# Kernel tuning notes

Hardware: AMD Instinct MI355X
Metric: run time of the kernel (lower is better)

The kernel has to match this reference:

```python
import math
import jax, jax.numpy as jnp
import numpy as np

E = 24  # num experts


def layer_norm(x, w, b, eps=1e-6):
    m = x.mean(-1, keepdims=True)
    v = x.var(-1, keepdims=True)
    return (x - m) / jnp.sqrt(v + eps) * w + b


def top2_dispatch(x, Wg, C):
    # x: [S, d] -> combine/dispatch: [S, E, C] (GShard/DeepSpeed top-2 gating)
    logits = x @ Wg                                   # [S, E]
    gates = jax.nn.softmax(logits, axis=-1)
    idx1 = jnp.argmax(gates, axis=-1)
    m1 = jax.nn.one_hot(idx1, E, dtype=x.dtype)       # [S, E]
    masked = jnp.where(m1 > 0, -jnp.inf, logits)
    idx2 = jnp.argmax(masked, axis=-1)
    m2 = jax.nn.one_hot(idx2, E, dtype=x.dtype)
    # position of each token within its expert's capacity buffer
    loc1 = jnp.cumsum(m1, axis=0) - m1
    loc2 = jnp.cumsum(m2, axis=0) - m2 + jnp.sum(m1, axis=0, keepdims=True)
    m1 = m1 * (loc1 < C)                              # drop overflow tokens
    m2 = m2 * (loc2 < C)
    g1 = jnp.sum(gates * m1, axis=-1)
    g2 = jnp.sum(gates * m2, axis=-1)
    denom = jnp.maximum(g1 + g2, 1e-9)
    g1, g2 = g1 / denom, g2 / denom
    p1 = jnp.sum(loc1 * m1, axis=-1).astype(jnp.int32)
    p2 = jnp.sum(loc2 * m2, axis=-1).astype(jnp.int32)
    c1 = g1[:, None, None] * m1[:, :, None] * jax.nn.one_hot(p1, C, dtype=x.dtype)[:, None, :]
    c2 = g2[:, None, None] * m2[:, :, None] * jax.nn.one_hot(p2, C, dtype=x.dtype)[:, None, :]
    combine = c1 + c2                                  # [S, E, C]
    dispatch = (combine > 0).astype(x.dtype)
    return combine, dispatch


def moe_apply(x, combine, dispatch, W, b):
    # dispatch tokens to expert buffers, per-expert GEMM, combine back
    disp = jnp.einsum('sec,sd->ecd', dispatch, x)      # [E, C, d]
    h = jnp.einsum('ecd,edf->ecf', disp, W) + b[:, None, :]
    return jnp.einsum('sec,ecf->sf', combine, h)       # [S, f]


def setup_inputs() -> dict:
    b, seq, d_in, d_hid = 4, 2048, 1024, 4096
    ks = jax.random.split(jax.random.key(0), 6)
    s = 0.02
    return {
        'x': jax.random.normal(ks[0], (b, seq, d_in), dtype=jnp.float32),
        'Wg': jax.random.normal(ks[1], (d_in, E), dtype=jnp.float32) * s,
        'W1': jax.random.normal(ks[2], (E, d_in, d_hid), dtype=jnp.float32) * s,
        'b1': jnp.zeros((E, d_hid), dtype=jnp.float32),
        'W2': jax.random.normal(ks[3], (E, d_hid, d_in), dtype=jnp.float32) * s,
        'b2': jnp.zeros((E, d_in), dtype=jnp.float32),
        'ln_hid_w': jnp.ones((4, d_hid), dtype=jnp.float32),
        'ln_hid_b': jnp.zeros((4, d_hid), dtype=jnp.float32),
        'ln_out_w': jnp.ones((d_in,), dtype=jnp.float32),
        'ln_out_b': jnp.zeros((d_in,), dtype=jnp.float32),
    }


def reference(x, Wg, W1, b1, W2, b2, ln_hid_w, ln_hid_b, ln_out_w, ln_out_b):
    bsz, seq, d = x.shape
    H = 4
    n = seq // H
    S = bsz * n  # tokens per sub-sequence MoE call
    C = math.ceil(2 * S / E)  # top-2 capacity, capacity_factor=1.0
    # b (h n) c -> h (b n) c
    xg = x.reshape(bsz, H, n, d).transpose(1, 0, 2, 3).reshape(H, S, d)

    def per_group(xf, lw, lb):
        combine, dispatch = top2_dispatch(xf, Wg, C)
        h = moe_apply(xf, combine, dispatch, W1, b1)       # [S, d_hid]
        h = layer_norm(h, lw, lb)
        h = jax.nn.relu(h)                                  # dropout = identity (eval)
        return moe_apply(h, combine, dispatch, W2, b2)      # reuse gate_decision

    out = jax.vmap(per_group)(xg, ln_hid_w, ln_hid_b)       # [H, S, d]
    out = out.reshape(H, bsz, n, d).transpose(1, 0, 2, 3).reshape(bsz, seq, d)
    return layer_norm(out + x, ln_out_w, ln_out_b)
```

## Files before the change

### kernel.cpp

```cpp
#include <hip/hip_runtime.h>
#include <cstdint>
#include <cstddef>

#define E_      24
#define D_IN    1024
#define D_HID   4096
#define HGRP    4
#define BSZ     4
#define SEQ     2048
#define NSUB    512
#define S_      2048
#define NTOKG   8192
#define CAP     171
#define MR      768
#define MTILE   3
#define KSPL2   4

typedef __attribute__((ext_vector_type(4))) float          f32x4;
typedef __attribute__((ext_vector_type(4))) unsigned short u16x4;
typedef __attribute__((ext_vector_type(8))) unsigned short u16x8;
typedef __attribute__((ext_vector_type(4))) unsigned int   u32x4;
typedef __attribute__((ext_vector_type(8))) short          s16x8;

__device__ __forceinline__ unsigned short f2bf(float f) {
  unsigned int u = __float_as_uint(f);
  u += 0x7fffu + ((u >> 16) & 1u);
  return (unsigned short)(u >> 16);
}
__device__ __forceinline__ float bf2f(unsigned short v) {
  return __uint_as_float(((unsigned int)v) << 16);
}

__global__ __launch_bounds__(64)
void k_gating(const float* __restrict__ x, const float* __restrict__ Wg,
              int* __restrict__ tokE1, int* __restrict__ tokE2,
              float* __restrict__ tokG1, float* __restrict__ tokG2) {
  int tg = blockIdx.x;
  int h = tg >> 11, s = tg & 2047;
  int bi = s >> 9, ni = s & 511;
  const float* xr = x + ((size_t)bi*SEQ + (size_t)h*NSUB + ni) * D_IN;
  int lane = threadIdx.x;
  float acc[E_];
  #pragma unroll
  for (int e = 0; e < E_; ++e) acc[e] = 0.f;
  #pragma unroll
  for (int it = 0; it < D_IN/256; ++it) {
    f32x4 xv = *(const f32x4*)(xr + it*256 + lane*4);
    #pragma unroll
    for (int j = 0; j < 4; ++j) {
      float xs = xv[j];
      const float* wrow = Wg + (size_t)(it*256 + lane*4 + j) * E_;
      #pragma unroll
      for (int e = 0; e < E_; ++e) acc[e] += xs * wrow[e];
    }
  }
  #pragma unroll
  for (int e = 0; e < E_; ++e) {
    float v = acc[e];
    v += __shfl_xor(v, 32); v += __shfl_xor(v, 16); v += __shfl_xor(v, 8);
    v += __shfl_xor(v, 4);  v += __shfl_xor(v, 2);  v += __shfl_xor(v, 1);
    acc[e] = v;
  }
  if (lane == 0) {
    float mx = acc[0];
    #pragma unroll
    for (int e = 1; e < E_; ++e) mx = fmaxf(mx, acc[e]);
    float den = 0.f;
    #pragma unroll
    for (int e = 0; e < E_; ++e) den += expf(acc[e] - mx);
    int i1 = 0; float v1 = acc[0];
    #pragma unroll
    for (int e = 1; e < E_; ++e) if (acc[e] > v1) { v1 = acc[e]; i1 = e; }
    int i2 = -1; float v2 = -3.4e38f;
    #pragma unroll
    for (int e = 0; e < E_; ++e) if (e != i1 && acc[e] > v2) { v2 = acc[e]; i2 = e; }
    tokE1[tg] = i1; tokE2[tg] = i2;
    tokG1[tg] = expf(v1 - mx) / den;
    tokG2[tg] = expf(v2 - mx) / den;
  }
}

__global__ void k_init_slots(int* __restrict__ slotTok) {
  slotTok[blockIdx.x*256 + threadIdx.x] = -1;
}

__global__ __launch_bounds__(64)
void k_scan(const int* __restrict__ tokE1, const int* __restrict__ tokE2,
            float* __restrict__ tokG1, float* __restrict__ tokG2,
            int* __restrict__ tokP1, int* __restrict__ tokP2,
            int* __restrict__ slotTok) {
  int h = blockIdx.x;
  int lane = threadIdx.x;
  __shared__ int cnt[64][E_];
  __shared__ int tot1[E_];
  const int CH = S_/64;
  const int* e1 = tokE1 + h*S_;
  const int* e2 = tokE2 + h*S_;
  #pragma unroll
  for (int e = 0; e < E_; ++e) cnt[lane][e] = 0;
  __syncthreads();
  for (int k = 0; k < CH; ++k) cnt[lane][e1[lane*CH + k]]++;
  __syncthreads();
  if (lane < E_) {
    int run = 0;
    for (int j = 0; j < 64; ++j) { int t = cnt[j][lane]; cnt[j][lane] = run; run += t; }
    tot1[lane] = run;
  }
  __syncthreads();
  for (int k = 0; k < CH; ++k) {
    int s = lane*CH + k;
    int e = e1[s];
    int p = cnt[lane][e]++;
    int tg = h*S_ + s;
    if (p < CAP) { tokP1[tg] = p; slotTok[e*MR + h*CAP + p] = tg; }
    else         { tokP1[tg] = -1; }
  }
  __syncthreads();
  #pragma unroll
  for (int e = 0; e < E_; ++e) cnt[lane][e] = 0;
  __syncthreads();
  for (int k = 0; k < CH; ++k) cnt[lane][e2[lane*CH + k]]++;
  __syncthreads();
  if (lane < E_) {
    int run = tot1[lane];
    for (int j = 0; j < 64; ++j) { int t = cnt[j][lane]; cnt[j][lane] = run; run += t; }
  }
  __syncthreads();
  for (int k = 0; k < CH; ++k) {
    int s = lane*CH + k;
    int e = e2[s];
    int p = cnt[lane][e]++;
    int tg = h*S_ + s;
    if (p < CAP) { tokP2[tg] = p; slotTok[e*MR + h*CAP + p] = tg; }
    else         { tokP2[tg] = -1; }
  }
  __syncthreads();
  for (int k = 0; k < CH; ++k) {
    int tg = h*S_ + k*64 + lane;
    float g1 = (tokP1[tg] >= 0) ? tokG1[tg] : 0.f;
    float g2 = (tokP2[tg] >= 0) ? tokG2[tg] : 0.f;
    float den = fmaxf(g1 + g2, 1e-9f);
    tokG1[tg] = g1 / den;
    tokG2[tg] = g2 / den;
  }
}

__global__ __launch_bounds__(256)
void k_gather1(const float* __restrict__ x, const int* __restrict__ slotTok,
               unsigned short* __restrict__ A1) {
  int row = blockIdx.x;
  int tok = slotTok[row];
  int t = threadIdx.x;
  int k = t*4;
  int ba = ((k & 63)*2) ^ ((row & 7) << 4);
  char* dst = (char*)A1 + (size_t)row*(D_IN*2) + (size_t)(k >> 6)*128 + ba;
  u16x4 pk;
  if (tok >= 0) {
    int h = tok >> 11, s = tok & 2047;
    int bi = s >> 9, ni = s & 511;
    const float* xr = x + ((size_t)bi*SEQ + (size_t)h*NSUB + ni) * D_IN;
    f32x4 v = *(const f32x4*)(xr + k);
    pk.x = f2bf(v.x); pk.y = f2bf(v.y); pk.z = f2bf(v.z); pk.w = f2bf(v.w);
  } else {
    pk.x = 0; pk.y = 0; pk.z = 0; pk.w = 0;
  }
  *(u16x4*)dst = pk;
}

template<int K, int N>
__global__ __launch_bounds__(256)
void k_cvtW(const float* __restrict__ W, unsigned short* __restrict__ Wt) {
  const int NB = N/64, KB = K/64;
  int bid = blockIdx.x;
  int kb = bid % KB;
  int rem = bid / KB;
  int nb = rem % NB;
  int e  = rem / NB;
  __shared__ float lds[64][65];
  int t = threadIdx.x;
  int rl = t >> 4;
  int cl = (t & 15) * 4;
  const float* base = W + ((size_t)e*K + (size_t)kb*64)*N + (size_t)nb*64;
  #pragma unroll
  for (int p = 0; p < 4; ++p) {
    int r = p*16 + rl;
    f32x4 v = *(const f32x4*)(base + (size_t)r*N + cl);
    lds[cl+0][r] = v.x; lds[cl+1][r] = v.y; lds[cl+2][r] = v.z; lds[cl+3][r] = v.w;
  }
  __syncthreads();
  int nl = t >> 2, kg = (t & 3) * 16;
  u16x8 c0, c1;
  #pragma unroll
  for (int j = 0; j < 8; ++j) {
    c0[j] = f2bf(lds[nl][kg + j]);
    c1[j] = f2bf(lds[nl][kg + 8 + j]);
  }
  char* dst = (char*)Wt + ((size_t)e*N + (size_t)nb*64 + nl)*(K*2) + (size_t)kb*128;
  int sw = (nl & 7) << 4;
  *(u16x8*)(dst + ((kg*2)      ^ sw)) = c0;
  *(u16x8*)(dst + ((kg*2 + 16) ^ sw)) = c1;
}

template<int KROW, int KCHUNK, int N>
__global__ __launch_bounds__(512, 2)
void k_gemm(const unsigned short* __restrict__ A, const unsigned short* __restrict__ Wt,
            const float* __restrict__ bias, unsigned short* __restrict__ Out) {
  const int NT = N / 256;
  const int KSPLIT = KROW / KCHUNK;
  const int NKT = KCHUNK / 64;
  int cpx = gridDim.x >> 3;
  int lb = blockIdx.x;
  int bid = (lb & 7) * cpx + (lb >> 3);
  int mt  = bid % MTILE;
  int rem = bid / MTILE;
  int kc  = rem % KSPLIT;
  rem /= KSPLIT;
  int nt  = rem % NT;
  int e   = rem / NT;

  const char* Ab = (const char*)A  + ((size_t)e*MR + (size_t)mt*256) * (KROW*2);
  const char* Bb = (const char*)Wt + ((size_t)e*N  + (size_t)nt*256) * (KROW*2);
  size_t kbase = (size_t)kc * (KCHUNK*2);

  __shared__ unsigned short As0[256*64];
  __shared__ unsigned short As1[256*64];
  __shared__ unsigned short Bs0[256*64];
  __shared__ unsigned short Bs1[256*64];

  int tid  = threadIdx.x;
  int lane = tid & 63;
  int wid  = tid >> 6;
  int wr = wid >> 2, wc = wid & 3;

  f32x4 acc[8][4];
  #pragma unroll
  for (int i = 0; i < 8; ++i)
    #pragma unroll
    for (int j = 0; j < 4; ++j) acc[i][j] = (f32x4)0.f;

  auto stageAi = [&](int kt2, unsigned short* As, int i) {
    size_t koff = kbase + (size_t)kt2*128;
    int L = i*8192 + tid*16;
    __builtin_amdgcn_global_load_lds(
        (const __attribute__((address_space(1))) void*)(Ab + (size_t)(L >> 7)*(KROW*2) + koff + (L & 127)),
        (__attribute__((address_space(3))) void*)((char*)As + L), 16, 0, 0);
  };
  auto stageBi = [&](int kt2, unsigned short* Bs, int i) {
    size_t koff = kbase + (size_t)kt2*128;
    int L = i*8192 + tid*16;
    __builtin_amdgcn_global_load_lds(
        (const __attribute__((address_space(1))) void*)(Bb + (size_t)(L >> 7)*(KROW*2) + koff + (L & 127)),
        (__attribute__((address_space(3))) void*)((char*)Bs + L), 16, 0, 0);
  };
  auto fragsA = [&](const unsigned short* As, int ra, int ks, s16x8* afr) {
    int kb = ks*64 + (lane >> 4)*16;
    #pragma unroll
    for (int i = 0; i < 4; ++i) {
      int r = wr*128 + ra*64 + i*16 + (lane & 15);
      afr[i] = *(const s16x8*)((const char*)As + r*128 + (kb ^ ((r & 7) << 4)));
    }
  };
  auto fragsB = [&](const unsigned short* Bs, int ks, s16x8* bfr) {
    int kb = ks*64 + (lane >> 4)*16;
    #pragma unroll
    for (int j = 0; j < 4; ++j) {
      int c = wc*64 + j*16 + (lane & 15);
      bfr[j] = *(const s16x8*)((const char*)Bs + c*128 + (kb ^ ((c & 7) << 4)));
    }
  };
  auto mfma16 = [&](int ra, const s16x8* afr, const s16x8* bfr) {
    __builtin_amdgcn_s_setprio(1);
    #pragma unroll
    for (int i = 0; i < 4; ++i)
      #pragma unroll
      for (int j = 0; j < 4; ++j)
        acc[ra*4+i][j] = __builtin_amdgcn_mfma_f32_16x16x32_bf16(afr[i], bfr[j], acc[ra*4+i][j], 0, 0, 0);
    __builtin_amdgcn_s_setprio(0);
  };

  unsigned short *Acur = As0, *Anxt = As1, *Bcur = Bs0, *Bnxt = Bs1;

  stageBi(0, Bcur, 0); stageBi(0, Bcur, 1); stageBi(0, Bcur, 2); stageBi(0, Bcur, 3);
  stageAi(0, Acur, 0); stageAi(0, Acur, 2);
  stageAi(0, Acur, 1); stageAi(0, Acur, 3);
  asm volatile("s_waitcnt vmcnt(2)" ::: "memory");
  __builtin_amdgcn_sched_barrier(0);
  __builtin_amdgcn_s_barrier();

  for (int kt = 0; kt < NKT; ++kt) {
    int tn = (kt + 1 < NKT) ? kt + 1 : kt;
    s16x8 afr[4], bfr[4];
    fragsA(Acur, 0, 0, afr); fragsB(Bcur, 0, bfr);
    stageBi(tn, Bnxt, 0); stageBi(tn, Bnxt, 1);
    asm volatile("s_waitcnt vmcnt(2)" ::: "memory");
    __builtin_amdgcn_sched_barrier(0);
    __builtin_amdgcn_s_barrier();
    asm volatile("s_waitcnt lgkmcnt(0)" ::: "memory");
    __builtin_amdgcn_sched_barrier(0);
    mfma16(0, afr, bfr);
    __builtin_amdgcn_s_barrier();
    fragsA(Acur, 1, 0, afr);
    stageBi(tn, Bnxt, 2); stageBi(tn, Bnxt, 3);
    __builtin_amdgcn_s_barrier();
    asm volatile("s_waitcnt lgkmcnt(0)" ::: "memory");
    __builtin_amdgcn_sched_barrier(0);
    mfma16(1, afr, bfr);
    __builtin_amdgcn_s_barrier();
    fragsA(Acur, 0, 1, afr); fragsB(Bcur, 1, bfr);
    stageAi(tn, Anxt, 0); stageAi(tn, Anxt, 2);
    __builtin_amdgcn_s_barrier();
    asm volatile("s_waitcnt lgkmcnt(0)" ::: "memory");
    __builtin_amdgcn_sched_barrier(0);
    mfma16(0, afr, bfr);
    __builtin_amdgcn_s_barrier();
    fragsA(Acur, 1, 1, afr);
    stageAi(tn, Anxt, 1); stageAi(tn, Anxt, 3);
    __builtin_amdgcn_s_barrier();
    asm volatile("s_waitcnt lgkmcnt(0)" ::: "memory");
    __builtin_amdgcn_sched_barrier(0);
    mfma16(1, afr, bfr);
    asm volatile("s_waitcnt vmcnt(2)" ::: "memory");
    __builtin_amdgcn_sched_barrier(0);
    __builtin_amdgcn_s_barrier();
    unsigned short* t1 = Acur; Acur = Anxt; Anxt = t1;
    unsigned short* t2 = Bcur; Bcur = Bnxt; Bnxt = t2;
  }

  unsigned short* Op = Out + (size_t)kc * ((size_t)E_*MR*N);
  #pragma unroll
  for (int j = 0; j < 4; ++j) {
    int col = nt*256 + wc*64 + j*16 + (lane & 15);
    float bv = (kc == 0) ? bias[(size_t)e*N + col] : 0.f;
    #pragma unroll
    for (int i = 0; i < 8; ++i) {
      int rowb = mt*256 + wr*128 + i*16 + (lane >> 4)*4;
      #pragma unroll
      for (int r = 0; r < 4; ++r) {
        float v = acc[i][j][r] + bv;
        Op[(size_t)e*MR*N + (size_t)(rowb + r)*N + col] = f2bf(v);
      }
    }
  }
}

__global__ __launch_bounds__(256)
void k_zero_empty(const int* __restrict__ slotTok, unsigned short* __restrict__ A2) {
  int row = blockIdx.x;
  if (slotTok[row] >= 0) return;
  u32x4 z = (u32x4)0u;
  char* base = (char*)A2 + (size_t)row*(D_HID*2) + threadIdx.x*32;
  *(u32x4*)base = z;
  *(u32x4*)(base + 16) = z;
}

__global__ __launch_bounds__(256)
void k_combine_ln(const unsigned short* __restrict__ H1,
                  const int* __restrict__ tokE1, const int* __restrict__ tokE2,
                  const int* __restrict__ tokP1, const int* __restrict__ tokP2,
                  const float* __restrict__ tokG1, const float* __restrict__ tokG2,
                  const float* __restrict__ lnw, const float* __restrict__ lnb,
                  unsigned short* __restrict__ A2) {
  int tg = blockIdx.x;
  int h = tg >> 11;
  int p1 = tokP1[tg], p2 = tokP2[tg];
  if (p1 < 0 && p2 < 0) return;
  float g1 = tokG1[tg], g2 = tokG2[tg];
  long r1 = (p1 >= 0) ? ((long)tokE1[tg]*MR + h*CAP + p1) : -1;
  long r2 = (p2 >= 0) ? ((long)tokE2[tg]*MR + h*CAP + p2) : -1;
  int t = threadIdx.x;
  float v[16];
  float sum = 0.f, sq = 0.f;
  #pragma unroll
  for (int u = 0; u < 4; ++u) {
    int f = u*1024 + t*4;
    float a0 = 0.f, a1 = 0.f, a2 = 0.f, a3 = 0.f;
    if (r1 >= 0) {
      u16x4 q = *(const u16x4*)(H1 + (size_t)r1*D_HID + f);
      a0 += g1*bf2f(q.x); a1 += g1*bf2f(q.y); a2 += g1*bf2f(q.z); a3 += g1*bf2f(q.w);
    }
    if (r2 >= 0) {
      u16x4 q = *(const u16x4*)(H1 + (size_t)r2*D_HID + f);
      a0 += g2*bf2f(q.x); a1 += g2*bf2f(q.y); a2 += g2*bf2f(q.z); a3 += g2*bf2f(q.w);
    }
    v[u*4+0] = a0; v[u*4+1] = a1; v[u*4+2] = a2; v[u*4+3] = a3;
    sum += a0 + a1 + a2 + a3;
    sq  += a0*a0 + a1*a1 + a2*a2 + a3*a3;
  }
  #pragma unroll
  for (int o = 32; o; o >>= 1) { sum += __shfl_xor(sum, o); sq += __shfl_xor(sq, o); }
  __shared__ float redA[4], redB[4];
  int wid = t >> 6;
  if ((t & 63) == 0) { redA[wid] = sum; redB[wid] = sq; }
  __syncthreads();
  float S = redA[0] + redA[1] + redA[2] + redA[3];
  float Q = redB[0] + redB[1] + redB[2] + redB[3];
  float m = S * (1.f / D_HID);
  float var = Q * (1.f / D_HID) - m*m;
  float rs = rsqrtf(var + 1e-6f);
  #pragma unroll
  for (int u = 0; u < 4; ++u) {
    int f = u*1024 + t*4;
    u16x4 pk;
    float y0 = fmaxf((v[u*4+0]-m)*rs*lnw[h*D_HID+f+0] + lnb[h*D_HID+f+0], 0.f);
    float y1 = fmaxf((v[u*4+1]-m)*rs*lnw[h*D_HID+f+1] + lnb[h*D_HID+f+1], 0.f);
    float y2 = fmaxf((v[u*4+2]-m)*rs*lnw[h*D_HID+f+2] + lnb[h*D_HID+f+2], 0.f);
    float y3 = fmaxf((v[u*4+3]-m)*rs*lnw[h*D_HID+f+3] + lnb[h*D_HID+f+3], 0.f);
    pk.x = f2bf(y0); pk.y = f2bf(y1); pk.z = f2bf(y2); pk.w = f2bf(y3);
    int chunk = f >> 6;
    int ob = (f & 63)*2;
    if (r1 >= 0)
      *(u16x4*)((char*)A2 + (size_t)r1*(D_HID*2) + (size_t)chunk*128 + (ob ^ (((int)r1 & 7) << 4))) = pk;
    if (r2 >= 0)
      *(u16x4*)((char*)A2 + (size_t)r2*(D_HID*2) + (size_t)chunk*128 + (ob ^ (((int)r2 & 7) << 4))) = pk;
  }
}

__global__ __launch_bounds__(256)
void k_final(const unsigned short* __restrict__ H2p, const float* __restrict__ x,
             const int* __restrict__ tokE1, const int* __restrict__ tokE2,
             const int* __restrict__ tokP1, const int* __restrict__ tokP2,
             const float* __restrict__ tokG1, const float* __restrict__ tokG2,
             const float* __restrict__ lnw, const float* __restrict__ lnb,
             float* __restrict__ out) {
  const size_t PSTR = (size_t)E_*MR*D_IN;
  int tg = blockIdx.x;
  int h = tg >> 11, s = tg & 2047;
  int bi = s >> 9, ni = s & 511;
  size_t xoff = ((size_t)bi*SEQ + (size_t)h*NSUB + ni) * D_IN;
  int p1 = tokP1[tg], p2 = tokP2[tg];
  float g1 = tokG1[tg], g2 = tokG2[tg];
  int t = threadIdx.x;
  int f = t*4;
  f32x4 xv = *(const f32x4*)(x + xoff + f);
  float v0 = xv.x, v1 = xv.y, v2 = xv.z, v3 = xv.w;
  if (p1 >= 0) {
    size_t r1 = (size_t)tokE1[tg]*MR + h*CAP + p1;
    float a0 = 0.f, a1 = 0.f, a2 = 0.f, a3 = 0.f;
    #pragma unroll
    for (int p = 0; p < KSPL2; ++p) {
      u16x4 q = *(const u16x4*)(H2p + p*PSTR + r1*D_IN + f);
      a0 += bf2f(q.x); a1 += bf2f(q.y); a2 += bf2f(q.z); a3 += bf2f(q.w);
    }
    v0 += g1*a0; v1 += g1*a1; v2 += g1*a2; v3 += g1*a3;
  }
  if (p2 >= 0) {
    size_t r2 = (size_t)tokE2[tg]*MR + h*CAP + p2;
    float a0 = 0.f, a1 = 0.f, a2 = 0.f, a3 = 0.f;
    #pragma unroll
    for (int p = 0; p < KSPL2; ++p) {
      u16x4 q = *(const u16x4*)(H2p + p*PSTR + r2*D_IN + f);
      a0 += bf2f(q.x); a1 += bf2f(q.y); a2 += bf2f(q.z); a3 += bf2f(q.w);
    }
    v0 += g2*a0; v1 += g2*a1; v2 += g2*a2; v3 += g2*a3;
  }
  float sum = v0+v1+v2+v3, sq = v0*v0+v1*v1+v2*v2+v3*v3;
  #pragma unroll
  for (int o = 32; o; o >>= 1) { sum += __shfl_xor(sum, o); sq += __shfl_xor(sq, o); }
  __shared__ float redA[4], redB[4];
  int wid = t >> 6;
  if ((t & 63) == 0) { redA[wid] = sum; redB[wid] = sq; }
  __syncthreads();
  float S = redA[0] + redA[1] + redA[2] + redA[3];
  float Q = redB[0] + redB[1] + redB[2] + redB[3];
  float m = S * (1.f / D_IN);
  float var = Q * (1.f / D_IN) - m*m;
  float rs = rsqrtf(var + 1e-6f);
  f32x4 res;
  res.x = (v0 - m)*rs*lnw[f+0] + lnb[f+0];
  res.y = (v1 - m)*rs*lnw[f+1] + lnb[f+1];
  res.z = (v2 - m)*rs*lnw[f+2] + lnb[f+2];
  res.w = (v3 - m)*rs*lnw[f+3] + lnb[f+3];
  *(f32x4*)(out + xoff + f) = res;
}

extern "C" void kernel_launch(void* const* d_in, const int* in_sizes, int n_in,
                              void* d_out, int out_size, void* d_ws, size_t ws_size,
                              hipStream_t stream) {
  const float* x    = (const float*)d_in[0];
  const float* Wg   = (const float*)d_in[1];
  const float* W1   = (const float*)d_in[2];
  const float* b1   = (const float*)d_in[3];
  const float* W2   = (const float*)d_in[4];
  const float* b2   = (const float*)d_in[5];
  const float* lnhw = (const float*)d_in[6];
  const float* lnhb = (const float*)d_in[7];
  const float* lnow = (const float*)d_in[8];
  const float* lnob = (const float*)d_in[9];
  float* out = (float*)d_out;
  (void)in_sizes; (void)n_in; (void)out_size; (void)ws_size;

  char* ws = (char*)d_ws;
  size_t off = 0;
  auto take = [&](size_t bytes) -> char* {
    char* p = ws + off;
    off += (bytes + 255) & ~(size_t)255;
    return p;
  };
  int*   tokE1 = (int*)take(NTOKG*sizeof(int));
  int*   tokE2 = (int*)take(NTOKG*sizeof(int));
  int*   tokP1 = (int*)take(NTOKG*sizeof(int));
  int*   tokP2 = (int*)take(NTOKG*sizeof(int));
  float* tokG1 = (float*)take(NTOKG*sizeof(float));
  float* tokG2 = (float*)take(NTOKG*sizeof(float));
  int*   slotTok = (int*)take((size_t)E_*MR*sizeof(int));
  unsigned short* A1 = (unsigned short*)take((size_t)E_*MR*D_IN*2);
  unsigned short* H1 = (unsigned short*)take((size_t)E_*MR*D_HID*2);
  unsigned short* A2 = (unsigned short*)take((size_t)E_*MR*D_HID*2);
  unsigned short* Wt = (unsigned short*)take((size_t)E_*D_IN*D_HID*2);
  unsigned short* H2p = H1;

  k_init_slots<<<dim3(E_*MR/256), dim3(256), 0, stream>>>(slotTok);
  k_gating<<<dim3(NTOKG), dim3(64), 0, stream>>>(x, Wg, tokE1, tokE2, tokG1, tokG2);
  k_scan<<<dim3(HGRP), dim3(64), 0, stream>>>(tokE1, tokE2, tokG1, tokG2, tokP1, tokP2, slotTok);
  k_gather1<<<dim3(E_*MR), dim3(256), 0, stream>>>(x, slotTok, A1);
  k_cvtW<D_IN, D_HID><<<dim3(E_*(D_HID/64)*(D_IN/64)), dim3(256), 0, stream>>>(W1, Wt);
  k_gemm<D_IN, D_IN, D_HID><<<dim3(E_*(D_HID/256)*MTILE), dim3(512), 0, stream>>>(A1, Wt, b1, H1);
  k_zero_empty<<<dim3(E_*MR), dim3(256), 0, stream>>>(slotTok, A2);
  k_combine_ln<<<dim3(NTOKG), dim3(256), 0, stream>>>(H1, tokE1, tokE2, tokP1, tokP2,
                                                      tokG1, tokG2, lnhw, lnhb, A2);
  k_cvtW<D_HID, D_IN><<<dim3(E_*(D_IN/64)*(D_HID/64)), dim3(256), 0, stream>>>(W2, Wt);
  k_gemm<D_HID, D_IN, D_IN><<<dim3(E_*(D_IN/256)*MTILE*KSPL2), dim3(512), 0, stream>>>(A2, Wt, b2, H2p);
  k_final<<<dim3(NTOKG), dim3(256), 0, stream>>>(H2p, x, tokE1, tokE2, tokP1, tokP2,
                                                 tokG1, tokG2, lnow, lnob, out);
}
```

Measured before the change: 875.5 us.

## Fuse fp32-to-bf16 weight conversion and transpose into GEMM B-tile staging

Removes the separate k_cvtW passes that converted and transposed W1/W2 into a bf16 workspace. The GEMM now loads fp32 weight rows into registers, converts them to bf16, and writes them transposed and swizzled into LDS. The aim is to avoid writing and rereading a 400MB-class intermediate and to drop two launches. In exchange, each M-tile block re-reads fp32 weights, so weight traffic roughly doubles per read and triples across MTILE blocks. It also adds register pressure (8 f32x4) and uses plain global loads instead of direct-to-LDS loads.

```diff
diff --git a/kernel.cpp b/kernel.cpp
--- a/kernel.cpp
+++ b/kernel.cpp
@@ -167,43 +167,9 @@
   *(u16x4*)dst = pk;
 }
 
-template<int K, int N>
-__global__ __launch_bounds__(256)
-void k_cvtW(const float* __restrict__ W, unsigned short* __restrict__ Wt) {
-  const int NB = N/64, KB = K/64;
-  int bid = blockIdx.x;
-  int kb = bid % KB;
-  int rem = bid / KB;
-  int nb = rem % NB;
-  int e  = rem / NB;
-  __shared__ float lds[64][65];
-  int t = threadIdx.x;
-  int rl = t >> 4;
-  int cl = (t & 15) * 4;
-  const float* base = W + ((size_t)e*K + (size_t)kb*64)*N + (size_t)nb*64;
-  #pragma unroll
-  for (int p = 0; p < 4; ++p) {
-    int r = p*16 + rl;
-    f32x4 v = *(const f32x4*)(base + (size_t)r*N + cl);
-    lds[cl+0][r] = v.x; lds[cl+1][r] = v.y; lds[cl+2][r] = v.z; lds[cl+3][r] = v.w;
-  }
-  __syncthreads();
-  int nl = t >> 2, kg = (t & 3) * 16;
-  u16x8 c0, c1;
-  #pragma unroll
-  for (int j = 0; j < 8; ++j) {
-    c0[j] = f2bf(lds[nl][kg + j]);
-    c1[j] = f2bf(lds[nl][kg + 8 + j]);
-  }
-  char* dst = (char*)Wt + ((size_t)e*N + (size_t)nb*64 + nl)*(K*2) + (size_t)kb*128;
-  int sw = (nl & 7) << 4;
-  *(u16x8*)(dst + ((kg*2)      ^ sw)) = c0;
-  *(u16x8*)(dst + ((kg*2 + 16) ^ sw)) = c1;
-}
-
 template<int KROW, int KCHUNK, int N>
 __global__ __launch_bounds__(512, 2)
-void k_gemm(const unsigned short* __restrict__ A, const unsigned short* __restrict__ Wt,
+void k_gemm(const unsigned short* __restrict__ A, const float* __restrict__ W,
             const float* __restrict__ bias, unsigned short* __restrict__ Out) {
   const int NT = N / 256;
   const int KSPLIT = KROW / KCHUNK;
@@ -218,8 +184,8 @@
   int nt  = rem % NT;
   int e   = rem / NT;
 
-  const char* Ab = (const char*)A  + ((size_t)e*MR + (size_t)mt*256) * (KROW*2);
-  const char* Bb = (const char*)Wt + ((size_t)e*N  + (size_t)nt*256) * (KROW*2);
+  const char*  Ab = (const char*)A + ((size_t)e*MR + (size_t)mt*256) * (KROW*2);
+  const float* We = W + (size_t)e*KROW*N + (size_t)nt*256;
   size_t kbase = (size_t)kc * (KCHUNK*2);
 
   __shared__ unsigned short As0[256*64];
@@ -238,6 +204,25 @@
     #pragma unroll
     for (int j = 0; j < 4; ++j) acc[i][j] = (f32x4)0.f;
 
+  int bn = ((tid >> 3) & 63) * 4;
+  int bk = (tid & 7) * 8;
+  f32x4 wv[8];
+
+  auto loadB = [&](int kt2) {
+    const float* p = We + (size_t)((size_t)kc*KCHUNK + (size_t)kt2*64 + bk)*N + bn;
+    #pragma unroll
+    for (int q = 0; q < 8; ++q) wv[q] = *(const f32x4*)(p + (size_t)q*N);
+  };
+  auto writeB = [&](unsigned short* Bs) {
+    #pragma unroll
+    for (int c = 0; c < 4; ++c) {
+      u16x8 col;
+      #pragma unroll
+      for (int q = 0; q < 8; ++q) col[q] = f2bf(wv[q][c]);
+      int n = bn + c;
+      *(u16x8*)((char*)Bs + n*128 + ((bk*2) ^ ((n & 7) << 4))) = col;
+    }
+  };
   auto stageAi = [&](int kt2, unsigned short* As, int i) {
     size_t koff = kbase + (size_t)kt2*128;
     int L = i*8192 + tid*16;
@@ -245,13 +230,6 @@
         (const __attribute__((address_space(1))) void*)(Ab + (size_t)(L >> 7)*(KROW*2) + koff + (L & 127)),
         (__attribute__((address_space(3))) void*)((char*)As + L), 16, 0, 0);
   };
-  auto stageBi = [&](int kt2, unsigned short* Bs, int i) {
-    size_t koff = kbase + (size_t)kt2*128;
-    int L = i*8192 + tid*16;
-    __builtin_amdgcn_global_load_lds(
-        (const __attribute__((address_space(1))) void*)(Bb + (size_t)(L >> 7)*(KROW*2) + koff + (L & 127)),
-        (__attribute__((address_space(3))) void*)((char*)Bs + L), 16, 0, 0);
-  };
   auto fragsA = [&](const unsigned short* As, int ra, int ks, s16x8* afr) {
     int kb = ks*64 + (lane >> 4)*16;
     #pragma unroll
@@ -280,48 +258,42 @@
 
   unsigned short *Acur = As0, *Anxt = As1, *Bcur = Bs0, *Bnxt = Bs1;
 
-  stageBi(0, Bcur, 0); stageBi(0, Bcur, 1); stageBi(0, Bcur, 2); stageBi(0, Bcur, 3);
-  stageAi(0, Acur, 0); stageAi(0, Acur, 2);
-  stageAi(0, Acur, 1); stageAi(0, Acur, 3);
-  asm volatile("s_waitcnt vmcnt(2)" ::: "memory");
-  __builtin_amdgcn_sched_barrier(0);
-  __builtin_amdgcn_s_barrier();
+  stageAi(0, Acur, 0); stageAi(0, Acur, 1); stageAi(0, Acur, 2); stageAi(0, Acur, 3);
+  loadB(0);
+  writeB(Bcur);
+  __syncthreads();
 
   for (int kt = 0; kt < NKT; ++kt) {
     int tn = (kt + 1 < NKT) ? kt + 1 : kt;
     s16x8 afr[4], bfr[4];
     fragsA(Acur, 0, 0, afr); fragsB(Bcur, 0, bfr);
-    stageBi(tn, Bnxt, 0); stageBi(tn, Bnxt, 1);
-    asm volatile("s_waitcnt vmcnt(2)" ::: "memory");
-    __builtin_amdgcn_sched_barrier(0);
+    loadB(tn);
     __builtin_amdgcn_s_barrier();
     asm volatile("s_waitcnt lgkmcnt(0)" ::: "memory");
     __builtin_amdgcn_sched_barrier(0);
     mfma16(0, afr, bfr);
     __builtin_amdgcn_s_barrier();
     fragsA(Acur, 1, 0, afr);
-    stageBi(tn, Bnxt, 2); stageBi(tn, Bnxt, 3);
+    stageAi(tn, Anxt, 0); stageAi(tn, Anxt, 2);
     __builtin_amdgcn_s_barrier();
     asm volatile("s_waitcnt lgkmcnt(0)" ::: "memory");
     __builtin_amdgcn_sched_barrier(0);
     mfma16(1, afr, bfr);
     __builtin_amdgcn_s_barrier();
     fragsA(Acur, 0, 1, afr); fragsB(Bcur, 1, bfr);
-    stageAi(tn, Anxt, 0); stageAi(tn, Anxt, 2);
+    stageAi(tn, Anxt, 1); stageAi(tn, Anxt, 3);
     __builtin_amdgcn_s_barrier();
     asm volatile("s_waitcnt lgkmcnt(0)" ::: "memory");
     __builtin_amdgcn_sched_barrier(0);
     mfma16(0, afr, bfr);
     __builtin_amdgcn_s_barrier();
     fragsA(Acur, 1, 1, afr);
-    stageAi(tn, Anxt, 1); stageAi(tn, Anxt, 3);
     __builtin_amdgcn_s_barrier();
     asm volatile("s_waitcnt lgkmcnt(0)" ::: "memory");
     __builtin_amdgcn_sched_barrier(0);
     mfma16(1, afr, bfr);
-    asm volatile("s_waitcnt vmcnt(2)" ::: "memory");
-    __builtin_amdgcn_sched_barrier(0);
-    __builtin_amdgcn_s_barrier();
+    writeB(Bnxt);
+    __syncthreads();
     unsigned short* t1 = Acur; Acur = Anxt; Anxt = t1;
     unsigned short* t2 = Bcur; Bcur = Bnxt; Bnxt = t2;
   }
@@ -506,20 +478,17 @@
   unsigned short* A1 = (unsigned short*)take((size_t)E_*MR*D_IN*2);
   unsigned short* H1 = (unsigned short*)take((size_t)E_*MR*D_HID*2);
   unsigned short* A2 = (unsigned short*)take((size_t)E_*MR*D_HID*2);
-  unsigned short* Wt = (unsigned short*)take((size_t)E_*D_IN*D_HID*2);
   unsigned short* H2p = H1;
 
   k_init_slots<<<dim3(E_*MR/256), dim3(256), 0, stream>>>(slotTok);
   k_gating<<<dim3(NTOKG), dim3(64), 0, stream>>>(x, Wg, tokE1, tokE2, tokG1, tokG2);
   k_scan<<<dim3(HGRP), dim3(64), 0, stream>>>(tokE1, tokE2, tokG1, tokG2, tokP1, tokP2, slotTok);
   k_gather1<<<dim3(E_*MR), dim3(256), 0, stream>>>(x, slotTok, A1);
-  k_cvtW<D_IN, D_HID><<<dim3(E_*(D_HID/64)*(D_IN/64)), dim3(256), 0, stream>>>(W1, Wt);
-  k_gemm<D_IN, D_IN, D_HID><<<dim3(E_*(D_HID/256)*MTILE), dim3(512), 0, stream>>>(A1, Wt, b1, H1);
+  k_gemm<D_IN, D_IN, D_HID><<<dim3(E_*(D_HID/256)*MTILE), dim3(512), 0, stream>>>(A1, W1, b1, H1);
   k_zero_empty<<<dim3(E_*MR), dim3(256), 0, stream>>>(slotTok, A2);
   k_combine_ln<<<dim3(NTOKG), dim3(256), 0, stream>>>(H1, tokE1, tokE2, tokP1, tokP2,
                                                       tokG1, tokG2, lnhw, lnhb, A2);
-  k_cvtW<D_HID, D_IN><<<dim3(E_*(D_IN/64)*(D_HID/64)), dim3(256), 0, stream>>>(W2, Wt);
-  k_gemm<D_HID, D_IN, D_IN><<<dim3(E_*(D_IN/256)*MTILE*KSPL2), dim3(512), 0, stream>>>(A2, Wt, b2, H2p);
+  k_gemm<D_HID, D_IN, D_IN><<<dim3(E_*(D_IN/256)*MTILE*KSPL2), dim3(512), 0, stream>>>(A2, W2, b2, H2p);
   k_final<<<dim3(NTOKG), dim3(256), 0, stream>>>(H2p, x, tokE1, tokE2, tokP1, tokP2,
                                                  tokG1, tokG2, lnow, lnob, out);
 }
```

Result: no change. 862.4 us (-1.5%).
